# Kernel tuning notes

Hardware: AMD Instinct MI355X
Metric: run time of the kernel (lower is better)

## Reference

```python
import jax, jax.numpy as jnp
import numpy as np

N_NODES = 50000
N_EDGES = 1600000
F_IN = 128
C = 64          # block in/out channels
EF = 64         # edge MLP hidden dim
BLOCKS = 3
MLP_DIM = 128
N_CLASSES = 10
N_GRAPHS = 512
EPS = 1e-5


def setup_inputs() -> dict:
    key = jax.random.key(0)
    ks = jax.random.split(key, 32)
    s = 0.05
    inp = {
        "x": jax.random.normal(ks[0], (N_NODES, F_IN), jnp.float32),
        "edge_index": jax.random.randint(ks[1], (2, N_EDGES), 0, N_NODES, jnp.int64),
        "batch": jnp.sort(jax.random.randint(ks[2], (N_NODES,), 0, N_GRAPHS, jnp.int64)),
        "fc0_w": jax.random.normal(ks[3], (F_IN, C), jnp.float32) * s,
        "fc0_b": jnp.zeros((C,), jnp.float32),
        "fc1_w": jax.random.normal(ks[4], (BLOCKS * C, MLP_DIM), jnp.float32) * s,
        "fc1_b": jnp.zeros((MLP_DIM,), jnp.float32),
        "fc2_w": jax.random.normal(ks[5], (MLP_DIM, N_CLASSES), jnp.float32) * s,
        "fc2_b": jnp.zeros((N_CLASSES,), jnp.float32),
    }
    for i in range(BLOCKS):
        k = 6 + 4 * i
        inp[f"bn_g{i}"] = jnp.ones((C,), jnp.float32)
        inp[f"bn_b{i}"] = jnp.zeros((C,), jnp.float32)
        inp[f"w1_{i}"] = jax.random.normal(ks[k], (2 * C, EF), jnp.float32) * s
        inp[f"b1_{i}"] = jnp.zeros((EF,), jnp.float32)
        inp[f"w2_{i}"] = jax.random.normal(ks[k + 1], (EF, C), jnp.float32) * s
        inp[f"b2_{i}"] = jnp.zeros((C,), jnp.float32)
    return inp


def _batchnorm(x, g, b):
    mu = jnp.mean(x, axis=0)
    var = jnp.var(x, axis=0)
    return (x - mu) * jax.lax.rsqrt(var + EPS) * g + b


def _edge_conv(x, src, dst, w1, b1, w2, b2):
    # PyG-style EdgeConv: msg = MLP(concat[x_i, x_j - x_i]), max-aggregate at i
    xi = x[dst]                                  # [E, C]
    xj = x[src]                                  # [E, C]
    h = jax.nn.relu(jnp.concatenate([xi, xj - xi], axis=-1) @ w1 + b1)  # [E, EF]
    m = h @ w2 + b2                              # [E, C]
    agg = jax.ops.segment_max(m, dst, num_segments=N_NODES)
    return jnp.where(jnp.isfinite(agg), agg, 0.0)


def reference(x, edge_index, batch, fc0_w, fc0_b, fc1_w, fc1_b, fc2_w, fc2_b,
              bn_g0, bn_b0, w1_0, b1_0, w2_0, b2_0,
              bn_g1, bn_b1, w1_1, b1_1, w2_1, b2_1,
              bn_g2, bn_b2, w1_2, b1_2, w2_2, b2_2):
    src, dst = edge_index[0], edge_index[1]
    h = x @ fc0_w + fc0_b                        # [N, C]
    blocks = [(bn_g0, bn_b0, w1_0, b1_0, w2_0, b2_0),
              (bn_g1, bn_b1, w1_1, b1_1, w2_1, b2_1),
              (bn_g2, bn_b2, w1_2, b1_2, w2_2, b2_2)]
    xs = []
    for (g, b, w1, b1, w2, b2) in blocks:
        h = _batchnorm(h, g, b)
        h = jax.nn.relu(_edge_conv(h, src, dst, w1, b1, w2, b2))
        xs.append(h)
    cat = jnp.concatenate(xs, axis=-1)           # [N, 3C]
    # global mean pool over graphs
    sums = jax.ops.segment_sum(cat, batch, num_segments=N_GRAPHS)
    cnt = jax.ops.segment_sum(jnp.ones((N_NODES,), cat.dtype), batch,
                              num_segments=N_GRAPHS)
    pooled = sums / jnp.maximum(cnt, 1.0)[:, None]   # [G, 3C]
    hid = jax.nn.relu(pooled @ fc1_w + fc1_b)
    return jax.nn.log_softmax(hid @ fc2_w + fc2_b, axis=-1)
```

## Files before the change

### kernel.cpp

```cpp
#include <hip/hip_runtime.h>
#include <math.h>

#define N_NODES 50000
#define N_TILES 3125
#define N_EDGES 1600000
#define F_IN 128
#define C 64
#define EF 64
#define N_GRAPHS 512
#define MLP_DIM 128
#define N_CLASSES 10
#define EPS 1e-5f
#define NB 196
#define CAPB 16384
#define CHUNK 4096
#define NPASS1 391
#define NFC0 782
#define NSLICE 8
#define EDGE_GRID 2048
#define SSTAGE 12288

typedef __attribute__((ext_vector_type(8))) _Float16 half8;
typedef __attribute__((ext_vector_type(2))) _Float16 half2v;
typedef __attribute__((ext_vector_type(4))) float floatx4;
typedef __attribute__((ext_vector_type(4))) unsigned uintx4;

union Uh { uintx4 v; half2v h[4]; half8 h8; };

__device__ __forceinline__ unsigned short f2h(float a) {
    union { _Float16 f; unsigned short u; } c;
    c.f = (_Float16)a;
    return c.u;
}
__device__ __forceinline__ float h2f(unsigned short u) {
    union { unsigned short u; _Float16 f; } c;
    c.u = u;
    return (float)c.f;
}
__device__ __forceinline__ half2v pk2(float a, float b) {
    auto t = __builtin_amdgcn_cvt_pkrtz(a, b);
    union { decltype(t) i; half2v o; } c;
    c.i = t;
    return c.o;
}

__global__ __launch_bounds__(256, 3) void fc0_pass1_kernel(
        const int* __restrict__ src, const int* __restrict__ dst,
        int* __restrict__ gcur, unsigned* __restrict__ keys,
        const float* __restrict__ x, const float* __restrict__ w,
        const float* __restrict__ b, unsigned short* __restrict__ h0,
        float* __restrict__ bns) {
    __shared__ int lcnt[NB], lbase[NB], lcnt2[NB];
    __shared__ float bl1[4][64], bl2[4][64];
    int tid = threadIdx.x;

    if (blockIdx.x < NPASS1) {
        int e0 = blockIdx.x * CHUNK;
        unsigned k[CHUNK / 256];
        int bk[CHUNK / 256];
        for (int i = tid; i < NB; i += 256) lcnt[i] = 0;
        __syncthreads();
#pragma unroll
        for (int i = 0; i < CHUNK / 256; i++) {
            int e = e0 + i * 256 + tid;
            if (e < N_EDGES) {
                int d = dst[e];
                k[i] = ((unsigned)d << 16) | (unsigned)src[e];
                bk[i] = d >> 8;
                atomicAdd(&lcnt[bk[i]], 1);
            } else bk[i] = -1;
        }
        __syncthreads();
        for (int i = tid; i < NB; i += 256) {
            int c = lcnt[i];
            lbase[i] = c ? atomicAdd(&gcur[i], c) : 0;
            lcnt2[i] = 0;
        }
        __syncthreads();
#pragma unroll
        for (int i = 0; i < CHUNK / 256; i++) {
            if (bk[i] >= 0) {
                int r = atomicAdd(&lcnt2[bk[i]], 1);
                keys[(size_t)bk[i] * CAPB + lbase[bk[i]] + r] = k[i];
            }
        }
        return;
    }

    int bid = blockIdx.x - NPASS1;
    int lane = tid & 63, wid = tid >> 6;
    int q = lane >> 4, cl = lane & 15, kq = q * 8;

    Uh wf[4][4];
#pragma unroll
    for (int kh = 0; kh < 4; kh++)
#pragma unroll
        for (int cb = 0; cb < 4; cb++)
#pragma unroll
            for (int j = 0; j < 4; j++) {
                int k0 = kh * 32 + kq + 2 * j;
                int col = cb * 16 + cl;
                wf[kh][cb].h[j] = pk2(w[k0 * 64 + col], w[(k0 + 1) * 64 + col]);
            }
    float bv[4];
#pragma unroll
    for (int cb = 0; cb < 4; cb++) bv[cb] = b[cb * 16 + cl];
    float s1[4] = {0, 0, 0, 0}, s2[4] = {0, 0, 0, 0};

    for (int t = bid * 4 + wid; t < N_TILES; t += NFC0 * 4) {
        int nb = t * 16;
        floatx4 acc[4] = {{0,0,0,0},{0,0,0,0},{0,0,0,0},{0,0,0,0}};
#pragma unroll
        for (int kh = 0; kh < 4; kh++) {
            const float* xr = x + (size_t)(nb + cl) * F_IN + kh * 32 + kq;
            floatx4 xa = *(const floatx4*)xr;
            floatx4 xb = *(const floatx4*)(xr + 4);
            Uh xf;
            xf.h[0] = pk2(xa.x, xa.y); xf.h[1] = pk2(xa.z, xa.w);
            xf.h[2] = pk2(xb.x, xb.y); xf.h[3] = pk2(xb.z, xb.w);
#pragma unroll
            for (int cb = 0; cb < 4; cb++)
                acc[cb] = __builtin_amdgcn_mfma_f32_16x16x32_f16(xf.h8, wf[kh][cb].h8, acc[cb], 0, 0, 0);
        }
#pragma unroll
        for (int cb = 0; cb < 4; cb++)
#pragma unroll
            for (int r = 0; r < 4; r++) {
                float v = acc[cb][r] + bv[cb];
                h0[(size_t)(nb + q * 4 + r) * 64 + cb * 16 + cl] = f2h(v);
                s1[cb] += v; s2[cb] += v * v;
            }
    }
#pragma unroll
    for (int cb = 0; cb < 4; cb++) {
        s1[cb] += __shfl_xor(s1[cb], 16); s1[cb] += __shfl_xor(s1[cb], 32);
        s2[cb] += __shfl_xor(s2[cb], 16); s2[cb] += __shfl_xor(s2[cb], 32);
    }
    if (lane < 16) {
#pragma unroll
        for (int cb = 0; cb < 4; cb++) { bl1[wid][cb * 16 + lane] = s1[cb]; bl2[wid][cb * 16 + lane] = s2[cb]; }
    }
    __syncthreads();
    if (tid < 64) {
        float a  = bl1[0][tid] + bl1[1][tid] + bl1[2][tid] + bl1[3][tid];
        float c2 = bl2[0][tid] + bl2[1][tid] + bl2[2][tid] + bl2[3][tid];
        int sl = bid & (NSLICE - 1);
        atomicAdd(&bns[sl * 128 + tid], a);
        atomicAdd(&bns[sl * 128 + 64 + tid], c2);
    }
}

__device__ __forceinline__ void ab_body(int bid, int tid,
                                        const unsigned short* __restrict__ h,
                                        const float* __restrict__ bns,
                                        const float* __restrict__ g,
                                        const float* __restrict__ bb,
                                        const float* __restrict__ w1,
                                        const float* __restrict__ b1,
                                        unsigned short* __restrict__ A,
                                        unsigned short* __restrict__ Bb,
                                        float* scale, float* shift, float* cab) {
    int lane = tid & 63, wid = tid >> 6;
    int q = lane >> 4, cl = lane & 15, kq = q * 8;

    if (tid < 64) {
        float s1v = 0.f, s2v = 0.f;
#pragma unroll
        for (int s = 0; s < NSLICE; s++) { s1v += bns[s * 128 + tid]; s2v += bns[s * 128 + 64 + tid]; }
        float mu  = s1v * (1.0f / N_NODES);
        float var = s2v * (1.0f / N_NODES) - mu * mu;
        float sc  = g[tid] * rsqrtf(var + EPS);
        scale[tid] = sc;
        shift[tid] = bb[tid] - mu * sc;
    }
    __syncthreads();
    if (tid < 128) {
        int j = tid & 63;
        float acc = (tid < 64) ? b1[j] : 0.f;
        for (int k = 0; k < 64; k++) {
            float wa_ = w1[k * EF + j], wb_ = w1[(64 + k) * EF + j];
            acc = fmaf(shift[k], (tid < 64) ? (wa_ - wb_) : wb_, acc);
        }
        cab[tid] = acc;
    }
    Uh wa[2][4], wb[2][4];
#pragma unroll
    for (int kh = 0; kh < 2; kh++)
#pragma unroll
        for (int cb = 0; cb < 4; cb++)
#pragma unroll
            for (int j = 0; j < 4; j++) {
                int k0 = kh * 32 + kq + 2 * j;
                int col = cb * 16 + cl;
                float sa = scale[k0], sb = scale[k0 + 1];
                float a0 = w1[k0 * EF + col], b0 = w1[(64 + k0) * EF + col];
                float a1 = w1[(k0 + 1) * EF + col], b1v = w1[(64 + k0 + 1) * EF + col];
                wa[kh][cb].h[j] = pk2(sa * (a0 - b0), sb * (a1 - b1v));
                wb[kh][cb].h[j] = pk2(sa * b0, sb * b1v);
            }
    __syncthreads();
    float cav[4], cbv[4];
#pragma unroll
    for (int cb = 0; cb < 4; cb++) { cav[cb] = cab[cb * 16 + cl]; cbv[cb] = cab[64 + cb * 16 + cl]; }

    for (int t = bid * 4 + wid; t < N_TILES; t += NFC0 * 4) {
        int nb = t * 16;
        const unsigned short* hrow = h + (size_t)(nb + cl) * 64 + kq;
        Uh h0f, h1f;
        h0f.v = *(const uintx4*)hrow;
        h1f.v = *(const uintx4*)(hrow + 32);
        floatx4 accA[4] = {{0,0,0,0},{0,0,0,0},{0,0,0,0},{0,0,0,0}};
        floatx4 accB[4] = {{0,0,0,0},{0,0,0,0},{0,0,0,0},{0,0,0,0}};
#pragma unroll
        for (int cb = 0; cb < 4; cb++) {
            accA[cb] = __builtin_amdgcn_mfma_f32_16x16x32_f16(h0f.h8, wa[0][cb].h8, accA[cb], 0, 0, 0);
            accB[cb] = __builtin_amdgcn_mfma_f32_16x16x32_f16(h0f.h8, wb[0][cb].h8, accB[cb], 0, 0, 0);
            accA[cb] = __builtin_amdgcn_mfma_f32_16x16x32_f16(h1f.h8, wa[1][cb].h8, accA[cb], 0, 0, 0);
            accB[cb] = __builtin_amdgcn_mfma_f32_16x16x32_f16(h1f.h8, wb[1][cb].h8, accB[cb], 0, 0, 0);
        }
#pragma unroll
        for (int cb = 0; cb < 4; cb++)
#pragma unroll
            for (int r = 0; r < 4; r++) {
                size_t o = (size_t)(nb + q * 4 + r) * 64 + cb * 16 + cl;
                A[o]  = f2h(accA[cb][r] + cav[cb]);
                Bb[o] = f2h(accB[cb][r] + cbv[cb]);
            }
    }
}

__global__ __launch_bounds__(256, 4) void sort2_ab_kernel(
        const unsigned* __restrict__ keys, const int* __restrict__ bcnt,
        int* __restrict__ cnt, int* __restrict__ gtotal,
        int* __restrict__ row_start, unsigned short* __restrict__ sorted_src,
        const unsigned short* __restrict__ h, const float* __restrict__ bns,
        const float* __restrict__ g, const float* __restrict__ bb,
        const float* __restrict__ w1, const float* __restrict__ b1,
        unsigned short* __restrict__ A, unsigned short* __restrict__ Bb) {
    __shared__ int lc[256], loc[256], lrs[256], cur[256];
    __shared__ int base;
    __shared__ float scale[64], shift[64], cab[128];
    __shared__ unsigned short sstage[SSTAGE];
    int tid = threadIdx.x;
    if (blockIdx.x < NB) {
        int b = blockIdx.x;
        lc[tid] = 0;
        cur[tid] = 0;
        __syncthreads();
        int nk = bcnt[b];
        const unsigned* kb = keys + (size_t)b * CAPB;
        for (int p = tid; p < nk; p += 256)
            atomicAdd(&lc[(kb[p] >> 16) & 255], 1);
        __syncthreads();
        int node = b * 256 + tid;
        int c = lc[tid];
        if (node < N_NODES) cnt[node] = c;
        int pc = (c + 15) & ~15;
        loc[tid] = pc;
        __syncthreads();
        for (int off = 1; off < 256; off <<= 1) {
            int t = (tid >= off) ? loc[tid - off] : 0;
            __syncthreads();
            loc[tid] += t;
            __syncthreads();
        }
        if (tid == 255) base = atomicAdd(gtotal, loc[255]);
        __syncthreads();
        int total = loc[255];
        int myl = loc[tid] - pc;
        lrs[tid] = myl;
        if (node < N_NODES) row_start[node] = base + myl;
        __syncthreads();
        if (total <= SSTAGE) {
            for (int p = tid; p < nk; p += 256) {
                unsigned k = kb[p];
                int lidx = (k >> 16) & 255;
                int r = atomicAdd(&cur[lidx], 1);
                sstage[lrs[lidx] + r] = (unsigned short)(k & 0xFFFFu);
            }
            __syncthreads();
            if (node < N_NODES && c > 0) {
                unsigned short s0 = sstage[myl];
                int pe = myl + pc;
                for (int p = myl + c; p < pe; p++) sstage[p] = s0;
            }
            __syncthreads();
            uintx4* d4 = (uintx4*)(sorted_src + base);
            const uintx4* s4 = (const uintx4*)sstage;
            int n4 = total >> 3;
            for (int j = tid; j < n4; j += 256) d4[j] = s4[j];
        } else {
            for (int p = tid; p < nk; p += 256) {
                unsigned k = kb[p];
                int lidx = (k >> 16) & 255;
                int r = atomicAdd(&cur[lidx], 1);
                sorted_src[base + lrs[lidx] + r] = (unsigned short)(k & 0xFFFFu);
            }
            __syncthreads();
            if (node < N_NODES && c > 0) {
                int g0 = base + myl;
                unsigned short s0 = sorted_src[g0];
                int pe = g0 + pc;
                for (int p = g0 + c; p < pe; p++) sorted_src[p] = s0;
            }
        }
        return;
    }
    ab_body(blockIdx.x - NB, tid, h, bns, g, bb, w1, b1, A, Bb, scale, shift, cab);
}

__global__ __launch_bounds__(256, 4) void ab_mfma_kernel(
        const unsigned short* __restrict__ h, const float* __restrict__ bns,
        const float* __restrict__ g, const float* __restrict__ bb,
        const float* __restrict__ w1, const float* __restrict__ b1,
        unsigned short* __restrict__ A, unsigned short* __restrict__ Bb) {
    __shared__ float scale[64], shift[64], cab[128];
    ab_body(blockIdx.x, threadIdx.x, h, bns, g, bb, w1, b1, A, Bb, scale, shift, cab);
}

__global__ __launch_bounds__(256, 4) void edge_mfma_kernel(
        const unsigned short* __restrict__ A, const unsigned short* __restrict__ Bb,
        const int* __restrict__ row_start, const int* __restrict__ cnt,
        const unsigned short* __restrict__ sorted_src,
        const float* __restrict__ w2, const float* __restrict__ b2,
        unsigned short* __restrict__ catp, float* __restrict__ bnsNext) {
    __shared__ float r1[4][64], r2[4][64];
    __shared__ unsigned short stage[4][2][1024];
    int tid = threadIdx.x, lane = tid & 63, wid = tid >> 6;
    int q = lane >> 4;
    int cl = lane & 15;
    int kq = q * 8;

    Uh bfr[2][4];
#pragma unroll
    for (int kh = 0; kh < 2; kh++)
#pragma unroll
        for (int cb = 0; cb < 4; cb++)
#pragma unroll
            for (int j = 0; j < 4; j++) {
                _Float16 w0 = (_Float16)w2[(kh * 32 + kq + 2 * j) * 64 + cb * 16 + cl];
                _Float16 w1v = (_Float16)w2[(kh * 32 + kq + 2 * j + 1) * 64 + cb * 16 + cl];
                bfr[kh][cb].h[j] = half2v{w0, w1v};
            }
    float b2j = b2[lane];
    float s1 = 0.f, s2 = 0.f;
    const half2v zeroh = {(_Float16)0.f, (_Float16)0.f};

    int srow = lane >> 3;
    int st   = lane & 7;
    int wswz = (st * 16) ^ (srow << 4);
    int woff0 = srow * 128 + wswz;
    int woff1 = (8 + srow) * 128 + wswz;
    int rswz  = (cl & 7) << 4;
    int roff0 = cl * 128 + ((q * 16) ^ rswz);
    int roff1 = cl * 128 + ((64 + q * 16) ^ rswz);

    char* mystage0 = (char*)&stage[wid][0][0];
    char* mystage1 = (char*)&stage[wid][1][0];

    for (int n = blockIdx.x * 4 + wid; n < N_NODES; n += gridDim.x * 4) {
        int beg = row_start[n];
        int end = beg + ((cnt[n] + 15) & ~15);
        const unsigned short* arow = A + (size_t)n * 64 + kq;
        Uh a0u, a1u;
        a0u.v = *(const uintx4*)(arow);
        a1u.v = *(const uintx4*)(arow + 32);
        floatx4 rmax0 = {-INFINITY, -INFINITY, -INFINITY, -INFINITY};
        floatx4 rmax1 = rmax0, rmax2 = rmax0, rmax3 = rmax0;

        auto stageTile = [&](int p, char* sb) {
            int s0 = (int)sorted_src[p + srow];
            int s1v = (int)sorted_src[p + 8 + srow];
            uintx4 v0 = *(const uintx4*)(Bb + (size_t)s0 * 64 + st * 8);
            uintx4 v1 = *(const uintx4*)(Bb + (size_t)s1v * 64 + st * 8);
            *(uintx4*)(sb + woff0) = v0;
            *(uintx4*)(sb + woff1) = v1;
        };
        auto tileLds = [&](const char* sb) {
            Uh b0u, b1u, f0, f1;
            b0u.v = *(const uintx4*)(sb + roff0);
            b1u.v = *(const uintx4*)(sb + roff1);
#pragma unroll
            for (int j = 0; j < 4; j++) {
                f0.h[j] = __builtin_elementwise_max(a0u.h[j] + b0u.h[j], zeroh);
                f1.h[j] = __builtin_elementwise_max(a1u.h[j] + b1u.h[j], zeroh);
            }
            floatx4 acc0 = {0.f, 0.f, 0.f, 0.f}, acc1 = acc0, acc2 = acc0, acc3 = acc0;
            acc0 = __builtin_amdgcn_mfma_f32_16x16x32_f16(f0.h8, bfr[0][0].h8, acc0, 0, 0, 0);
            acc1 = __builtin_amdgcn_mfma_f32_16x16x32_f16(f0.h8, bfr[0][1].h8, acc1, 0, 0, 0);
            acc2 = __builtin_amdgcn_mfma_f32_16x16x32_f16(f0.h8, bfr[0][2].h8, acc2, 0, 0, 0);
            acc3 = __builtin_amdgcn_mfma_f32_16x16x32_f16(f0.h8, bfr[0][3].h8, acc3, 0, 0, 0);
            acc0 = __builtin_amdgcn_mfma_f32_16x16x32_f16(f1.h8, bfr[1][0].h8, acc0, 0, 0, 0);
            acc1 = __builtin_amdgcn_mfma_f32_16x16x32_f16(f1.h8, bfr[1][1].h8, acc1, 0, 0, 0);
            acc2 = __builtin_amdgcn_mfma_f32_16x16x32_f16(f1.h8, bfr[1][2].h8, acc2, 0, 0, 0);
            acc3 = __builtin_amdgcn_mfma_f32_16x16x32_f16(f1.h8, bfr[1][3].h8, acc3, 0, 0, 0);
            rmax0 = __builtin_elementwise_max(rmax0, acc0);
            rmax1 = __builtin_elementwise_max(rmax1, acc1);
            rmax2 = __builtin_elementwise_max(rmax2, acc2);
            rmax3 = __builtin_elementwise_max(rmax3, acc3);
        };

        int p0 = beg;
        for (; p0 + 32 <= end; p0 += 32) {
            stageTile(p0, mystage0);
            stageTile(p0 + 16, mystage1);
            tileLds(mystage0);
            tileLds(mystage1);
        }
        if (p0 < end) {
            stageTile(p0, mystage0);
            tileLds(mystage0);
        }

        float v0 = fmaxf(fmaxf(rmax0.x, rmax0.y), fmaxf(rmax0.z, rmax0.w));
        float v1 = fmaxf(fmaxf(rmax1.x, rmax1.y), fmaxf(rmax1.z, rmax1.w));
        float v2 = fmaxf(fmaxf(rmax2.x, rmax2.y), fmaxf(rmax2.z, rmax2.w));
        float v3 = fmaxf(fmaxf(rmax3.x, rmax3.y), fmaxf(rmax3.z, rmax3.w));
        v0 = fmaxf(v0, __shfl_xor(v0, 16)); v0 = fmaxf(v0, __shfl_xor(v0, 32));
        v1 = fmaxf(v1, __shfl_xor(v1, 16)); v1 = fmaxf(v1, __shfl_xor(v1, 32));
        v2 = fmaxf(v2, __shfl_xor(v2, 16)); v2 = fmaxf(v2, __shfl_xor(v2, 32));
        v3 = fmaxf(v3, __shfl_xor(v3, 16)); v3 = fmaxf(v3, __shfl_xor(v3, 32));
        float vs = (lane & 32) ? ((lane & 16) ? v3 : v2) : ((lane & 16) ? v1 : v0);
        float v = fmaxf(vs + b2j, 0.f);
        catp[(size_t)n * 64 + lane] = f2h(v);
        s1 += v; s2 += v * v;
    }

    if (bnsNext) {
        r1[wid][lane] = s1; r2[wid][lane] = s2;
        __syncthreads();
        if (tid < 64) {
            float a  = r1[0][tid] + r1[1][tid] + r1[2][tid] + r1[3][tid];
            float c2 = r2[0][tid] + r2[1][tid] + r2[2][tid] + r2[3][tid];
            int sl = blockIdx.x & (NSLICE - 1);
            atomicAdd(&bnsNext[sl * 128 + tid], a);
            atomicAdd(&bnsNext[sl * 128 + 64 + tid], c2);
        }
    }
}

__global__ __launch_bounds__(192) void poolhead_kernel(const unsigned short* __restrict__ cat0,
                                                       const unsigned short* __restrict__ cat1,
                                                       const unsigned short* __restrict__ cat2,
                                                       const int* __restrict__ batch,
                                                       const float* __restrict__ fc1w,
                                                       const float* __restrict__ fc1b,
                                                       const float* __restrict__ fc2w,
                                                       const float* __restrict__ fc2b,
                                                       float* __restrict__ out) {
    __shared__ int se[2];
    __shared__ float p[192];
    __shared__ float hid[128];
    __shared__ float z[10];
    __shared__ float lse;
    int g = blockIdx.x, tid = threadIdx.x;
    if (tid < 2) {
        int target = g + tid;
        int lo = 0, hi = N_NODES;
        while (lo < hi) { int mid = (lo + hi) >> 1; if (batch[mid] < target) lo = mid + 1; else hi = mid; }
        se[tid] = lo;
    }
    __syncthreads();
    int s = se[0], e = se[1];
    const unsigned short* plane = (tid < 64) ? cat0 : ((tid < 128) ? cat1 : cat2);
    int col = tid & 63;
    float a0 = 0.f, a1 = 0.f, a2 = 0.f, a3 = 0.f;
    int r = s;
    for (; r + 4 <= e; r += 4) {
        a0 += h2f(plane[(size_t)(r + 0) * 64 + col]);
        a1 += h2f(plane[(size_t)(r + 1) * 64 + col]);
        a2 += h2f(plane[(size_t)(r + 2) * 64 + col]);
        a3 += h2f(plane[(size_t)(r + 3) * 64 + col]);
    }
    for (; r < e; r++) a0 += h2f(plane[(size_t)r * 64 + col]);
    float acc = (a0 + a1) + (a2 + a3);
    float denom = (e > s) ? (float)(e - s) : 1.0f;
    p[tid] = acc / denom;
    __syncthreads();
    if (tid < MLP_DIM) {
        float a = fc1b[tid];
        for (int k = 0; k < 192; k++) a = fmaf(p[k], fc1w[k * 128 + tid], a);
        hid[tid] = fmaxf(a, 0.f);
    }
    __syncthreads();
    if (tid < N_CLASSES) {
        float a = fc2b[tid];
        for (int k = 0; k < 128; k++) a = fmaf(hid[k], fc2w[k * 10 + tid], a);
        z[tid] = a;
    }
    __syncthreads();
    if (tid == 0) {
        float m = z[0];
        for (int i = 1; i < 10; i++) m = fmaxf(m, z[i]);
        float sm = 0.f;
        for (int i = 0; i < 10; i++) sm += expf(z[i] - m);
        lse = m + logf(sm);
    }
    __syncthreads();
    if (tid < N_CLASSES) out[g * 10 + tid] = z[tid] - lse;
}

extern "C" void kernel_launch(void* const* d_in, const int* in_sizes, int n_in,
                              void* d_out, int out_size, void* d_ws, size_t ws_size,
                              hipStream_t stream) {
    (void)in_sizes; (void)n_in; (void)out_size; (void)ws_size;
    const float* x    = (const float*)d_in[0];
    const int*   ei   = (const int*)d_in[1];
    const int*   batch= (const int*)d_in[2];
    const float* fc0w = (const float*)d_in[3];
    const float* fc0b = (const float*)d_in[4];
    const float* fc1w = (const float*)d_in[5];
    const float* fc1b = (const float*)d_in[6];
    const float* fc2w = (const float*)d_in[7];
    const float* fc2b = (const float*)d_in[8];
    const int* src = ei;
    const int* dst = ei + N_EDGES;
    float* out = (float*)d_out;

    char* w = (char*)d_ws;
    size_t off = 0;
    auto alloc = [&](size_t bytes) -> void* {
        void* p = w + off;
        off = (off + bytes + 255) & ~(size_t)255;
        return p;
    };
    const size_t MAX_PAD_EDGES = (size_t)N_EDGES + 16 * (size_t)N_NODES;

    const size_t BNS_OFF = 1280;
    const size_t ZBYTES  = BNS_OFF + 3 * NSLICE * 128 * 4;
    char* zbase = (char*)alloc(ZBYTES);
    int*   gcur   = (int*)zbase;
    int*   gtotal = (int*)(zbase + 1024);
    float* bnsAll = (float*)(zbase + BNS_OFF);

    unsigned short* cat0 = (unsigned short*)alloc((size_t)N_NODES * 64 * 2);
    unsigned short* cat1 = (unsigned short*)alloc((size_t)N_NODES * 64 * 2);
    unsigned short* cat2 = (unsigned short*)alloc((size_t)N_NODES * 64 * 2);
    unsigned short* h0   = (unsigned short*)alloc((size_t)N_NODES * 64 * 2);
    unsigned short* Ae   = (unsigned short*)alloc((size_t)N_NODES * 64 * 2);
    unsigned short* Be   = (unsigned short*)alloc((size_t)N_NODES * 64 * 2);
    unsigned* keys = (unsigned*)alloc((size_t)NB * CAPB * 4);
    unsigned short* sorted_src = (unsigned short*)alloc(MAX_PAD_EDGES * 2);
    int*   cnt       = (int*)alloc((size_t)N_NODES * 4);
    int*   row_start = (int*)alloc((size_t)N_NODES * 4);

    (void)hipMemsetAsync(zbase, 0, ZBYTES, stream);

    fc0_pass1_kernel<<<NPASS1 + NFC0, 256, 0, stream>>>(src, dst, gcur, keys,
                                                        x, fc0w, fc0b, h0, bnsAll);
    sort2_ab_kernel<<<NB + NFC0, 256, 0, stream>>>(
        keys, gcur, cnt, gtotal, row_start, sorted_src,
        h0, bnsAll,
        (const float*)d_in[9], (const float*)d_in[10],
        (const float*)d_in[11], (const float*)d_in[12], Ae, Be);

    unsigned short* planes[3] = {cat0, cat1, cat2};
    for (int blk = 0; blk < 3; blk++) {
        const float* w2 = (const float*)d_in[13 + 6 * blk];
        const float* b2 = (const float*)d_in[14 + 6 * blk];
        if (blk > 0) {
            ab_mfma_kernel<<<NFC0, 256, 0, stream>>>(
                planes[blk - 1], bnsAll + blk * NSLICE * 128,
                (const float*)d_in[9 + 6 * blk], (const float*)d_in[10 + 6 * blk],
                (const float*)d_in[11 + 6 * blk], (const float*)d_in[12 + 6 * blk], Ae, Be);
        }
        edge_mfma_kernel<<<EDGE_GRID, 256, 0, stream>>>(
            Ae, Be, row_start, cnt, sorted_src, w2, b2, planes[blk],
            (blk < 2) ? (bnsAll + (blk + 1) * NSLICE * 128) : nullptr);
    }

    poolhead_kernel<<<N_GRAPHS, 192, 0, stream>>>(cat0, cat1, cat2, batch,
                                                  fc1w, fc1b, fc2w, fc2b, out);
}
```

Before: 359.0 us.

## Software-pipeline edge gathers across nodes with register prefetch and triple LDS staging

Restructures the per-node edge loop into a cross-iteration pipeline. Row metadata is fetched two nodes ahead, source indices one node ahead, and the first three 16-edge tiles of B rows for the next node are held in registers. These are written into three LDS stage buffers before compute, so the global gather latency overlaps the MFMA work of the previous node. This costs more registers, which may reduce occupancy under launch_bounds(256,4), and more LDS. Nodes with more than 48 edges fall back to an unpipelined per-tile loop.

Result: slower. 438.3 us (+22.1%).

```diff
diff --git a/kernel.cpp b/kernel.cpp
--- a/kernel.cpp
+++ b/kernel.cpp
@@ -325,7 +325,7 @@
         const float* __restrict__ w2, const float* __restrict__ b2,
         unsigned short* __restrict__ catp, float* __restrict__ bnsNext) {
     __shared__ float r1[4][64], r2[4][64];
-    __shared__ unsigned short stage[4][2][1024];
+    __shared__ unsigned short stage[4][3][1024];
     int tid = threadIdx.x, lane = tid & 63, wid = tid >> 6;
     int q = lane >> 4;
     int cl = lane & 15;
@@ -355,27 +355,65 @@
     int roff0 = cl * 128 + ((q * 16) ^ rswz);
     int roff1 = cl * 128 + ((64 + q * 16) ^ rswz);
 
-    char* mystage0 = (char*)&stage[wid][0][0];
-    char* mystage1 = (char*)&stage[wid][1][0];
-
-    for (int n = blockIdx.x * 4 + wid; n < N_NODES; n += gridDim.x * 4) {
-        int beg = row_start[n];
-        int end = beg + ((cnt[n] + 15) & ~15);
+    char* sb0 = (char*)&stage[wid][0][0];
+    char* sb1 = (char*)&stage[wid][1][0];
+    char* sb2 = (char*)&stage[wid][2][0];
+
+    const int S = EDGE_GRID * 4;
+    int n = blockIdx.x * 4 + wid;
+
+    int rs0 = 0, ct0 = 0;
+    int rs1 = 0, ct1 = 0;
+    int sn0 = 0, sn1 = 0, sn2 = 0, sn3 = 0, sn4 = 0, sn5 = 0;
+    uintx4 x0 = {0,0,0,0}, x1 = x0, y0 = x0, y1 = x0, z0 = x0, z1 = x0;
+
+    auto bload = [&](int s, uintx4& u) {
+        u = *(const uintx4*)(Bb + (size_t)s * 64 + st * 8);
+    };
+
+    if (n < N_NODES) {
+        rs0 = row_start[n]; ct0 = cnt[n];
+        int nn = n + S;
+        if (nn < N_NODES) { rs1 = row_start[nn]; ct1 = cnt[nn]; }
+        int nt0 = (ct0 + 15) >> 4;
+        if (nt0 > 0) { int a = sorted_src[rs0 + srow],      b = sorted_src[rs0 + 8 + srow];  bload(a, x0); bload(b, x1); }
+        if (nt0 > 1) { int a = sorted_src[rs0 + 16 + srow], b = sorted_src[rs0 + 24 + srow]; bload(a, y0); bload(b, y1); }
+        if (nt0 > 2) { int a = sorted_src[rs0 + 32 + srow], b = sorted_src[rs0 + 40 + srow]; bload(a, z0); bload(b, z1); }
+        if (nn < N_NODES) {
+            int nt1 = (ct1 + 15) >> 4;
+            if (nt1 > 0) { sn0 = sorted_src[rs1 + srow];      sn1 = sorted_src[rs1 + 8 + srow]; }
+            if (nt1 > 1) { sn2 = sorted_src[rs1 + 16 + srow]; sn3 = sorted_src[rs1 + 24 + srow]; }
+            if (nt1 > 2) { sn4 = sorted_src[rs1 + 32 + srow]; sn5 = sorted_src[rs1 + 40 + srow]; }
+        }
+    }
+
+    while (n < N_NODES) {
+        int begC = rs0, cC = ct0;
+        int ntC = (cC + 15) >> 4;
+        int nn = n + S, nn2 = n + 2 * S;
+
+        int rs2 = 0, ct2 = 0;
+        if (nn2 < N_NODES) { rs2 = row_start[nn2]; ct2 = cnt[nn2]; }
+
         const unsigned short* arow = A + (size_t)n * 64 + kq;
         Uh a0u, a1u;
         a0u.v = *(const uintx4*)(arow);
         a1u.v = *(const uintx4*)(arow + 32);
+
+        if (ntC > 0) { *(uintx4*)(sb0 + woff0) = x0; *(uintx4*)(sb0 + woff1) = x1; }
+        if (ntC > 1) { *(uintx4*)(sb1 + woff0) = y0; *(uintx4*)(sb1 + woff1) = y1; }
+        if (ntC > 2) { *(uintx4*)(sb2 + woff0) = z0; *(uintx4*)(sb2 + woff1) = z1; }
+
+        if (nn < N_NODES) {
+            int nt1 = (ct1 + 15) >> 4;
+            if (nt1 > 0) { bload(sn0, x0); bload(sn1, x1); }
+            if (nt1 > 1) { bload(sn2, y0); bload(sn3, y1); }
+            if (nt1 > 2) { bload(sn4, z0); bload(sn5, z1); }
+        }
+
         floatx4 rmax0 = {-INFINITY, -INFINITY, -INFINITY, -INFINITY};
         floatx4 rmax1 = rmax0, rmax2 = rmax0, rmax3 = rmax0;
 
-        auto stageTile = [&](int p, char* sb) {
-            int s0 = (int)sorted_src[p + srow];
-            int s1v = (int)sorted_src[p + 8 + srow];
-            uintx4 v0 = *(const uintx4*)(Bb + (size_t)s0 * 64 + st * 8);
-            uintx4 v1 = *(const uintx4*)(Bb + (size_t)s1v * 64 + st * 8);
-            *(uintx4*)(sb + woff0) = v0;
-            *(uintx4*)(sb + woff1) = v1;
-        };
         auto tileLds = [&](const char* sb) {
             Uh b0u, b1u, f0, f1;
             b0u.v = *(const uintx4*)(sb + roff0);
@@ -400,16 +438,18 @@
             rmax3 = __builtin_elementwise_max(rmax3, acc3);
         };
 
-        int p0 = beg;
-        for (; p0 + 32 <= end; p0 += 32) {
-            stageTile(p0, mystage0);
-            stageTile(p0 + 16, mystage1);
-            tileLds(mystage0);
-            tileLds(mystage1);
-        }
-        if (p0 < end) {
-            stageTile(p0, mystage0);
-            tileLds(mystage0);
+        if (ntC > 0) tileLds(sb0);
+        if (ntC > 1) tileLds(sb1);
+        if (ntC > 2) tileLds(sb2);
+
+        for (int t = 3; t < ntC; t++) {
+            int pa = sorted_src[begC + t * 16 + srow];
+            int pb = sorted_src[begC + t * 16 + 8 + srow];
+            uintx4 u0, u1;
+            bload(pa, u0); bload(pb, u1);
+            *(uintx4*)(sb0 + woff0) = u0;
+            *(uintx4*)(sb0 + woff1) = u1;
+            tileLds(sb0);
         }
 
         float v0 = fmaxf(fmaxf(rmax0.x, rmax0.y), fmaxf(rmax0.z, rmax0.w));
@@ -424,6 +464,16 @@
         float v = fmaxf(vs + b2j, 0.f);
         catp[(size_t)n * 64 + lane] = f2h(v);
         s1 += v; s2 += v * v;
+
+        if (nn2 < N_NODES) {
+            int nt2 = (ct2 + 15) >> 4;
+            if (nt2 > 0) { sn0 = sorted_src[rs2 + srow];      sn1 = sorted_src[rs2 + 8 + srow]; }
+            if (nt2 > 1) { sn2 = sorted_src[rs2 + 16 + srow]; sn3 = sorted_src[rs2 + 24 + srow]; }
+            if (nt2 > 2) { sn4 = sorted_src[rs2 + 32 + srow]; sn5 = sorted_src[rs2 + 40 + srow]; }
+        }
+
+        rs0 = rs1; ct0 = ct1; rs1 = rs2; ct1 = ct2;
+        n = nn;
     }
 
     if (bnsNext) {
```
